# Optimization experiments

Measured on AMD Instinct MI355X. Metric: run time of the kernel, lower is better.

## Reference

```python
import jax, jax.numpy as jnp
import numpy as np

GAMMA = 0.9
TEMPERATURE = 0.07
BASE_TEMPERATURE = 0.07
U_SIZE = 15_000_000
BSZ, N_VIEWS, DIM = 2048, 2, 256


def setup_inputs() -> dict:
    key = jax.random.key(0)
    kf, = jax.random.split(key, 1)
    feats = jax.random.normal(kf, (BSZ, N_VIEWS, DIM), dtype=jnp.float32)
    # contrastive features are unit-normalized in practice
    feats = feats / jnp.linalg.norm(feats, axis=-1, keepdims=True)
    index = jnp.arange(BSZ, dtype=jnp.int64) if jax.config.jax_enable_x64 else jnp.arange(BSZ, dtype=jnp.int32)
    u = jnp.zeros((U_SIZE, 1), dtype=jnp.float32)
    return {"index": index, "features": feats, "u": u}


def reference(index, features, u):
    B, V, D = features.shape          # bsz, n_views, dim
    N = B * V
    eye_b = jnp.eye(B, dtype=jnp.float32)

    # torch.cat(torch.unbind(features, dim=1), dim=0) -> [V*B, D], views stacked
    contrast_feature = jnp.transpose(features, (1, 0, 2)).reshape(N, D)
    anchor_feature = contrast_feature  # contrast_mode == 'all'

    # [N, N] similarity logits
    anchor_dot_contrast = jnp.matmul(anchor_feature, contrast_feature.T) / TEMPERATURE
    logits_max = jax.lax.stop_gradient(jnp.max(anchor_dot_contrast, axis=1, keepdims=True))
    logits = anchor_dot_contrast - logits_max

    # positive mask: tiled identity with self-contrast removed
    mask = jnp.tile(eye_b, (V, V))
    logits_mask = 1.0 - jnp.eye(N, dtype=jnp.float32)  # scatter of zeros on the diagonal
    pos_mask = mask * logits_mask
    neg_mask = 1.0 - pos_mask

    # detached negative exp-logits (EMA statistics)
    neg_exp_logits = jax.lax.stop_gradient(jnp.exp(logits) * neg_mask)

    # indexed EMA buffer update: u[index] = (1-g)*u[index] + g*rowsum[:B]
    row_sum = jnp.sum(neg_exp_logits, axis=1, keepdims=True)[:B]   # [B, 1]
    u_new = (1.0 - GAMMA) * u[index] + GAMMA * row_sum             # [B, 1]
    # (buffer write: u = u.at[index].set(u_new); only u_new is read below)

    p_neg_pairs = neg_exp_logits / jnp.tile(u_new, (V, 1))         # [N, N], detached numer/denom
    log_prob = logits - jnp.sum(p_neg_pairs * logits * neg_mask, axis=1, keepdims=True)

    mean_log_prob_pos = jnp.sum(pos_mask * log_prob, axis=1) / jnp.sum(pos_mask, axis=1)
    loss = -(TEMPERATURE / BASE_TEMPERATURE) * mean_log_prob_pos
    return loss.reshape(V, B).mean()
```

## Files before the change

### kernel.cpp

```cpp
#include <hip/hip_runtime.h>


#define BSZ   2048
#define NROW  4096
#define DDIM  256
#define INVT  (1.0f / 0.07f)
#define NB64  64
#define NT2   (NB64 * (NB64 + 1) / 2)
#define TPB   4
#define NBLK  (NT2 / TPB)

typedef __attribute__((ext_vector_type(8))) __bf16 bf16x8;
typedef __attribute__((ext_vector_type(4))) float f32x4;

__device__ __forceinline__ short f2bs(float x) {
    __bf16 b = (__bf16)x;
    return __builtin_bit_cast(short, b);
}

__device__ __forceinline__ const float* crow_ptr(const float* feats, int i) {
    return feats + (((i & (BSZ - 1)) * 2 + (i >> 11)) << 8);
}

__global__ __launch_bounds__(256) void prep_kernel(const float* __restrict__ feats,
        float* __restrict__ selfdot, float* __restrict__ EWzero,
        short* __restrict__ CmF) {
    int tid = threadIdx.x;
    int z = blockIdx.x * 256 + tid;
    if (z < 2 * NROW) EWzero[z] = 0.0f;

    int lane = tid & 63;
    int row  = (blockIdx.x << 2) + (tid >> 6);
    const float4* src = (const float4*)crow_ptr(feats, row);
    float4 v = src[lane];
    float a0 = (float)(__bf16)v.x, a1 = (float)(__bf16)v.y;
    float a2 = (float)(__bf16)v.z, a3 = (float)(__bf16)v.w;
    float s = a0 * a0 + a1 * a1 + a2 * a2 + a3 * a3;
    #pragma unroll
    for (int off = 32; off; off >>= 1) s += __shfl_xor(s, off, 64);
    if (lane == 0) selfdot[row] = s;

    int gid  = z;
    int quad = gid & 3;
    int l15  = (gid >> 2) & 15;
    int rt   = (gid >> 6) & 3;
    int k    = (gid >> 8) & 7;
    int b    = gid >> 12;
    int srow = (b << 6) + (rt << 4) + l15;
    int kel  = (k << 5) + (quad << 3);
    const float4* fp = (const float4*)(crow_ptr(feats, srow) + kel);
    float4 v0 = fp[0], v1 = fp[1];
    short h[8] = { f2bs(v0.x), f2bs(v0.y), f2bs(v0.z), f2bs(v0.w),
                   f2bs(v1.x), f2bs(v1.y), f2bs(v1.z), f2bs(v1.w) };
    *(int4*)(CmF + gid * 8) = *(int4*)h;
}

__global__ __launch_bounds__(256, 2) void gemm_sym(const short* __restrict__ CmF,
        const float* __restrict__ selfdot, float* __restrict__ E,
        float* __restrict__ W, float* __restrict__ Lpos) {
    int tid  = threadIdx.x;
    int wave = tid >> 6;
    int lane = tid & 63;
    int quad = lane >> 4;
    int l15  = lane & 15;

    int t = blockIdx.x * TPB + wave;
    int p = (int)((sqrtf(8.0f * (float)t + 1.0f) - 1.0f) * 0.5f);
    while ((p + 1) * (p + 2) / 2 <= t) ++p;
    while (p * (p + 1) / 2 > t) --p;
    int q = t - p * (p + 1) / 2;
    int rowBase = q << 6;
    int colBase = p << 6;
    bool offdiag = (p != q);

    const short* aB = CmF + q * 16384 + ((l15 << 2) + quad) * 8;
    const short* bB = CmF + p * 16384 + ((l15 << 2) + quad) * 8;

    f32x4 acc[4][4];
    #pragma unroll
    for (int a = 0; a < 4; ++a)
        #pragma unroll
        for (int c = 0; c < 4; ++c) acc[a][c] = (f32x4){0.f, 0.f, 0.f, 0.f};

    bf16x8 aC[4], bC[4];
    #pragma unroll
    for (int rt = 0; rt < 4; ++rt) aC[rt] = *(const bf16x8*)(aB + rt * 512);
    #pragma unroll
    for (int ct = 0; ct < 4; ++ct) bC[ct] = *(const bf16x8*)(bB + ct * 512);

    #pragma unroll
    for (int k = 0; k < 8; ++k) {
        bf16x8 aN[4], bN[4];
        if (k < 7) {
            #pragma unroll
            for (int rt = 0; rt < 4; ++rt)
                aN[rt] = *(const bf16x8*)(aB + ((k + 1) * 4 + rt) * 512);
            #pragma unroll
            for (int ct = 0; ct < 4; ++ct)
                bN[ct] = *(const bf16x8*)(bB + ((k + 1) * 4 + ct) * 512);
        }
        #pragma unroll
        for (int rt = 0; rt < 4; ++rt)
            #pragma unroll
            for (int ct = 0; ct < 4; ++ct)
                acc[rt][ct] = __builtin_amdgcn_mfma_f32_16x16x32_bf16(
                    aC[rt], bC[ct], acc[rt][ct], 0, 0, 0);
        if (k < 7) {
            #pragma unroll
            for (int rt = 0; rt < 4; ++rt) aC[rt] = aN[rt];
            #pragma unroll
            for (int ct = 0; ct < 4; ++ct) bC[ct] = bN[ct];
        }
    }

    float sdr[4][4];
    #pragma unroll
    for (int rt = 0; rt < 4; ++rt)
        #pragma unroll
        for (int r = 0; r < 4; ++r)
            sdr[rt][r] = selfdot[rowBase + rt * 16 + (quad << 2) + r];
    float sdc[4];
    #pragma unroll
    for (int ct = 0; ct < 4; ++ct)
        sdc[ct] = selfdot[colBase + ct * 16 + l15];

    float Ep[4][4] = {}, Wp[4][4] = {};
    float Ec[4] = {}, Wc[4] = {};
    #pragma unroll
    for (int rt = 0; rt < 4; ++rt) {
        #pragma unroll
        for (int ct = 0; ct < 4; ++ct) {
            int gcol = colBase + ct * 16 + l15;
            #pragma unroll
            for (int r = 0; r < 4; ++r) {
                int grow = rowBase + rt * 16 + (quad << 2) + r;
                float d = acc[rt][ct][r];
                float l = (d - sdr[rt][r]) * INVT;
                float e = __expf(l);
                Ep[rt][r] += e;
                Wp[rt][r] += e * l;
                if (gcol == (grow ^ BSZ)) Lpos[grow] = l;
                if (offdiag) {
                    float l2 = (d - sdc[ct]) * INVT;
                    float e2 = __expf(l2);
                    Ec[ct] += e2;
                    Wc[ct] += e2 * l2;
                    if (grow == (gcol ^ BSZ)) Lpos[gcol] = l2;
                }
            }
        }
    }
    #pragma unroll
    for (int rt = 0; rt < 4; ++rt) {
        #pragma unroll
        for (int r = 0; r < 4; ++r) {
            float e = Ep[rt][r], w = Wp[rt][r];
            #pragma unroll
            for (int off = 1; off < 16; off <<= 1) {
                e += __shfl_xor(e, off, 64);
                w += __shfl_xor(w, off, 64);
            }
            if (l15 == 0) {
                int grow = rowBase + rt * 16 + (quad << 2) + r;
                atomicAdd(&E[grow], e);
                atomicAdd(&W[grow], w);
            }
        }
    }
    if (offdiag) {
        #pragma unroll
        for (int ct = 0; ct < 4; ++ct) {
            float e = Ec[ct], w = Wc[ct];
            e += __shfl_xor(e, 16, 64);  w += __shfl_xor(w, 16, 64);
            e += __shfl_xor(e, 32, 64);  w += __shfl_xor(w, 32, 64);
            if (quad == 0) {
                int gcol = colBase + ct * 16 + l15;
                atomicAdd(&E[gcol], e);
                atomicAdd(&W[gcol], w);
            }
        }
    }
}

__global__ __launch_bounds__(1024) void finalize_kernel(const int* __restrict__ index,
        const float* __restrict__ u, const float* __restrict__ E,
        const float* __restrict__ W, const float* __restrict__ Lpos,
        float* __restrict__ out) {
    __shared__ float unew[BSZ];
    __shared__ float partial[16];
    int tid = threadIdx.x;
    for (int b = tid; b < BSZ; b += 1024) {
        float lp = Lpos[b];
        unew[b] = 0.1f * u[index[b]] + 0.9f * (E[b] - __expf(lp));
    }
    __syncthreads();
    float local = 0.0f;
    for (int i = tid; i < NROW; i += 1024) {
        float lp  = Lpos[i];
        float elp = __expf(lp);
        local += lp - (W[i] - elp * lp) / unew[i & (BSZ - 1)];
    }
    #pragma unroll
    for (int off = 32; off; off >>= 1) local += __shfl_xor(local, off, 64);
    if ((tid & 63) == 0) partial[tid >> 6] = local;
    __syncthreads();
    if (tid == 0) {
        float s = 0.0f;
        #pragma unroll
        for (int w = 0; w < 16; ++w) s += partial[w];
        out[0] = -s / (float)NROW;
    }
}

extern "C" void kernel_launch(void* const* d_in, const int* in_sizes, int n_in,
                              void* d_out, int out_size, void* d_ws, size_t ws_size,
                              hipStream_t stream) {
    const int*   index = (const int*)d_in[0];
    const float* feats = (const float*)d_in[1];
    const float* u     = (const float*)d_in[2];
    float* out = (float*)d_out;

    float* selfdot = (float*)d_ws;
    float* E    = selfdot + NROW;
    float* W    = E + NROW;
    float* Lpos = W + NROW;
    short* CmF  = (short*)((char*)d_ws + 131072);

    prep_kernel<<<1024, 256, 0, stream>>>(feats, selfdot, E, CmF);
    gemm_sym<<<NBLK, 256, 0, stream>>>(CmF, selfdot, E, W, Lpos);
    finalize_kernel<<<1, 1024, 0, stream>>>(index, u, E, W, Lpos, out);
}
```

Baseline: 116.2 us.

## Launch one wave per tile block and deepen register prefetch to three stages

The symmetric GEMM kernel now runs one 64-thread block per triangular tile instead of packing four waves per 256-thread block, giving 2080 small blocks. The operand fragments are loaded into a three-deep register ring, two k-steps ahead, instead of double buffering with copies. The aim is finer-grained scheduling and more latency hiding for the global loads feeding the MFMAs. The cost is higher register pressure, and with launch_bounds(64,2) single-wave blocks could limit occupancy per CU.

```diff
diff --git a/kernel.cpp b/kernel.cpp
--- a/kernel.cpp
+++ b/kernel.cpp
@@ -7,8 +7,6 @@
 #define INVT  (1.0f / 0.07f)
 #define NB64  64
 #define NT2   (NB64 * (NB64 + 1) / 2)
-#define TPB   4
-#define NBLK  (NT2 / TPB)
 
 typedef __attribute__((ext_vector_type(8))) __bf16 bf16x8;
 typedef __attribute__((ext_vector_type(4))) float f32x4;
@@ -55,16 +53,14 @@
     *(int4*)(CmF + gid * 8) = *(int4*)h;
 }
 
-__global__ __launch_bounds__(256, 2) void gemm_sym(const short* __restrict__ CmF,
+__global__ __launch_bounds__(64, 2) void gemm_sym(const short* __restrict__ CmF,
         const float* __restrict__ selfdot, float* __restrict__ E,
         float* __restrict__ W, float* __restrict__ Lpos) {
-    int tid  = threadIdx.x;
-    int wave = tid >> 6;
-    int lane = tid & 63;
+    int lane = threadIdx.x;
     int quad = lane >> 4;
     int l15  = lane & 15;
 
-    int t = blockIdx.x * TPB + wave;
+    int t = blockIdx.x;
     int p = (int)((sqrtf(8.0f * (float)t + 1.0f) - 1.0f) * 0.5f);
     while ((p + 1) * (p + 2) / 2 <= t) ++p;
     while (p * (p + 1) / 2 > t) --p;
@@ -82,35 +78,35 @@
         #pragma unroll
         for (int c = 0; c < 4; ++c) acc[a][c] = (f32x4){0.f, 0.f, 0.f, 0.f};
 
-    bf16x8 aC[4], bC[4];
-    #pragma unroll
-    for (int rt = 0; rt < 4; ++rt) aC[rt] = *(const bf16x8*)(aB + rt * 512);
-    #pragma unroll
-    for (int ct = 0; ct < 4; ++ct) bC[ct] = *(const bf16x8*)(bB + ct * 512);
+    bf16x8 aF[3][4], bF[3][4];
+    #pragma unroll
+    for (int rt = 0; rt < 4; ++rt) {
+        aF[0][rt] = *(const bf16x8*)(aB + (0 * 4 + rt) * 512);
+        bF[0][rt] = *(const bf16x8*)(bB + (0 * 4 + rt) * 512);
+    }
+    #pragma unroll
+    for (int rt = 0; rt < 4; ++rt) {
+        aF[1][rt] = *(const bf16x8*)(aB + (1 * 4 + rt) * 512);
+        bF[1][rt] = *(const bf16x8*)(bB + (1 * 4 + rt) * 512);
+    }
 
     #pragma unroll
     for (int k = 0; k < 8; ++k) {
-        bf16x8 aN[4], bN[4];
-        if (k < 7) {
-            #pragma unroll
-            for (int rt = 0; rt < 4; ++rt)
-                aN[rt] = *(const bf16x8*)(aB + ((k + 1) * 4 + rt) * 512);
-            #pragma unroll
-            for (int ct = 0; ct < 4; ++ct)
-                bN[ct] = *(const bf16x8*)(bB + ((k + 1) * 4 + ct) * 512);
+        int cur = k % 3;
+        int nxt = (k + 2) % 3;
+        if (k < 6) {
+            #pragma unroll
+            for (int rt = 0; rt < 4; ++rt) {
+                aF[nxt][rt] = *(const bf16x8*)(aB + ((k + 2) * 4 + rt) * 512);
+                bF[nxt][rt] = *(const bf16x8*)(bB + ((k + 2) * 4 + rt) * 512);
+            }
         }
         #pragma unroll
         for (int rt = 0; rt < 4; ++rt)
             #pragma unroll
             for (int ct = 0; ct < 4; ++ct)
                 acc[rt][ct] = __builtin_amdgcn_mfma_f32_16x16x32_bf16(
-                    aC[rt], bC[ct], acc[rt][ct], 0, 0, 0);
-        if (k < 7) {
-            #pragma unroll
-            for (int rt = 0; rt < 4; ++rt) aC[rt] = aN[rt];
-            #pragma unroll
-            for (int ct = 0; ct < 4; ++ct) bC[ct] = bN[ct];
-        }
+                    aF[cur][rt], bF[cur][ct], acc[rt][ct], 0, 0, 0);
     }
 
     float sdr[4][4];
@@ -227,6 +223,6 @@
     short* CmF  = (short*)((char*)d_ws + 131072);
 
     prep_kernel<<<1024, 256, 0, stream>>>(feats, selfdot, E, CmF);
-    gemm_sym<<<NBLK, 256, 0, stream>>>(CmF, selfdot, E, W, Lpos);
+    gemm_sym<<<NT2, 64, 0, stream>>>(CmF, selfdot, E, W, Lpos);
     finalize_kernel<<<1, 1024, 0, stream>>>(index, u, E, W, Lpos, out);
 }
```

Result: no change. 116.6 us (+0.4%).
